# Kernel tuning notes

Measured on AMD Instinct MI355X. Metric: run time of the kernel, lower is better.

## Reference

```python
import jax, jax.numpy as jnp
import numpy as np

B, T, D, M = 2048, 512, 8, 2  # groups, timesteps, state_rank, n_measures


def setup_inputs() -> dict:
    key = jax.random.key(0)
    ks = jax.random.split(key, 7)
    inp = jax.random.normal(ks[0], (B, T, M), dtype=jnp.float32)
    mean0 = 0.1 * jax.random.normal(ks[1], (B, D), dtype=jnp.float32)
    A = 0.1 * jax.random.normal(ks[2], (B, D, D), dtype=jnp.float32)
    cov0 = A @ jnp.swapaxes(A, -1, -2) + jnp.eye(D, dtype=jnp.float32)  # PSD initial cov
    F = 0.95 * jnp.eye(D, dtype=jnp.float32) + 0.01 * jax.random.normal(ks[3], (D, D), dtype=jnp.float32)
    H = jax.random.normal(ks[4], (M, D), dtype=jnp.float32)
    Aq = 0.1 * jax.random.normal(ks[5], (D, D), dtype=jnp.float32)
    Q = Aq @ Aq.T + 0.1 * jnp.eye(D, dtype=jnp.float32)
    Ar = 0.1 * jax.random.normal(ks[6], (M, M), dtype=jnp.float32)
    R = Ar @ Ar.T + 0.1 * jnp.eye(M, dtype=jnp.float32)
    return dict(input=inp, mean0=mean0, cov0=cov0, F=F, H=H, Q=Q, R=R)


def _kf_scan(input, mean0, cov0, F, H, Q, R):
    """n_step=1 Kalman recurrence: at t emit the 1-step-ahead prediction made
    from data up to t-1 (so output[0] is the initial state), matching
    ScriptKalmanFilter.forward with n_step=1."""

    def step(carry, x_t):
        mean, cov = carry  # [B,D], [B,D,D]
        # --- update ---
        HP = jnp.einsum('md,bde->bme', H, cov)                 # H P : [B,M,D]
        S = jnp.einsum('bme,ne->bmn', HP, H) + R               # innovation cov [B,M,M]
        Kt = jnp.linalg.solve(S, HP)                           # K^T = S^{-1} H P : [B,M,D]
        resid = x_t - jnp.einsum('md,bd->bm', H, mean)         # [B,M]
        mean_u = mean + jnp.einsum('bmd,bm->bd', Kt, resid)
        cov_u = cov - jnp.einsum('bmd,bme->bde', Kt, HP)       # (I-KH)P
        # --- predict ---
        mean_p = jnp.einsum('de,be->bd', F, mean_u)
        cov_p = jnp.einsum('de,bef,gf->bdg', F, cov_u, F) + Q  # F P F^T + Q
        return (mean_p, cov_p), (mean_p, cov_p)

    xs = jnp.swapaxes(input, 0, 1)  # [T,B,M]
    _, (means_s, covs_s) = jax.lax.scan(step, (mean0, cov0), xs)
    # output at step t is the state BEFORE consuming x_t (1-step-ahead)
    means = jnp.concatenate([mean0[None], means_s[:-1]], axis=0)  # [T,B,D]
    covs = jnp.concatenate([cov0[None], covs_s[:-1]], axis=0)     # [T,B,D,D]
    return jnp.swapaxes(means, 0, 1), jnp.swapaxes(covs, 0, 1)


def reference(input, mean0, cov0, F, H, Q, R):
    means, covs = _kf_scan(input, mean0, cov0, F, H, Q, R)
    b, t, m = input.shape
    Rs = jnp.broadcast_to(R, (b, t, m, m))      # stacked per-time R (static design)
    Hs = jnp.broadcast_to(H, (b, t, m, H.shape[-1]))
    return means, covs, Rs, Hs
```

## Files before the change

### kernel.cpp

```cpp
#include <hip/hip_runtime.h>

typedef float v2 __attribute__((ext_vector_type(2)));
typedef float v4 __attribute__((ext_vector_type(4)));

#define B_TOT 2048
#define T_STEPS 512

#define OFF_COVS 8388608
#define OFF_RS   75497472
#define OFF_HS   79691776

__launch_bounds__(64, 1)
__global__ void kf_kernel(const float* __restrict__ input,
                          const float* __restrict__ mean0,
                          const float* __restrict__ cov0,
                          const float* __restrict__ Fm,
                          const float* __restrict__ Hm,
                          const float* __restrict__ Qm,
                          const float* __restrict__ Rm,
                          float* __restrict__ out)
{
    __shared__ float xs[8 * 1024];
    __shared__ float hp0_s[8 * 12];
    __shared__ float hp1_s[8 * 12];
    __shared__ float mean_s[8 * 12];
    __shared__ float u_s[8 * 88];

    const int lane = threadIdx.x;
    const int g = lane >> 3;
    const int j = lane & 7;
    const int b0 = blockIdx.x * 8;
    const int b = b0 + g;

    {
        const v4* src = (const v4*)(input + (size_t)b0 * 1024);
        v4* dst = (v4*)xs;
        #pragma unroll
        for (int i = 0; i < 32; ++i)
            dst[i * 64 + lane] = src[i * 64 + lane];
    }

    v2 Fcol2[8][4];
    #pragma unroll
    for (int f = 0; f < 8; ++f)
        #pragma unroll
        for (int d2 = 0; d2 < 4; ++d2) {
            v2 t; t.x = Fm[(2 * d2) * 8 + f]; t.y = Fm[(2 * d2 + 1) * 8 + f];
            Fcol2[f][d2] = t;
        }
    v2 Frowj[4];
    #pragma unroll
    for (int d2 = 0; d2 < 4; ++d2) {
        v2 t; t.x = Fm[j * 8 + 2 * d2]; t.y = Fm[j * 8 + 2 * d2 + 1];
        Frowj[d2] = t;
    }
    v2 Hrow2[2][4];
    #pragma unroll
    for (int m = 0; m < 2; ++m)
        #pragma unroll
        for (int d2 = 0; d2 < 4; ++d2) {
            v2 t; t.x = Hm[m * 8 + 2 * d2]; t.y = Hm[m * 8 + 2 * d2 + 1];
            Hrow2[m][d2] = t;
        }
    v2 HFrow2[2][4];
    #pragma unroll
    for (int m = 0; m < 2; ++m)
        #pragma unroll
        for (int d2 = 0; d2 < 4; ++d2) {
            float a = 0.f, c = 0.f;
            #pragma unroll
            for (int k = 0; k < 8; ++k) {
                a += Hm[m * 8 + k] * Fm[k * 8 + 2 * d2];
                c += Hm[m * 8 + k] * Fm[k * 8 + 2 * d2 + 1];
            }
            v2 t; t.x = a; t.y = c; HFrow2[m][d2] = t;
        }
    v2 Qrow2[4];
    #pragma unroll
    for (int e2 = 0; e2 < 4; ++e2) {
        v2 t; t.x = Qm[j * 8 + 2 * e2]; t.y = Qm[j * 8 + 2 * e2 + 1];
        Qrow2[e2] = t;
    }
    const float r00 = Rm[0], r01 = Rm[1], r10 = Rm[2], r11 = Rm[3];
    const float Rval = (j == 0) ? r00 : (j == 1) ? r01 : (j == 2) ? r10 : r11;
    v2 Hflat; Hflat.x = Hm[2 * j]; Hflat.y = Hm[2 * j + 1];

    v2 P2[4];
    {
        const v4* c4 = (const v4*)(cov0 + (size_t)b * 64 + j * 8);
        v4 a = c4[0], bb = c4[1];
        P2[0].x = a.x;  P2[0].y = a.y;  P2[1].x = a.z;  P2[1].y = a.w;
        P2[2].x = bb.x; P2[2].y = bb.y; P2[3].x = bb.z; P2[3].y = bb.w;
    }
    float mean_j = mean0[(size_t)b * 8 + j];

    float hm0, hm1;
    mean_s[g * 12 + j] = mean_j;
    __syncthreads();
    {
        const v4* ms = (const v4*)(mean_s + g * 12);
        v4 a = ms[0], bb = ms[1];
        v2 mu[4];
        mu[0].x = a.x;  mu[0].y = a.y;  mu[1].x = a.z;  mu[1].y = a.w;
        mu[2].x = bb.x; mu[2].y = bb.y; mu[3].x = bb.z; mu[3].y = bb.w;
        v2 t0 = {0.f, 0.f}, t1 = {0.f, 0.f};
        #pragma unroll
        for (int d2 = 0; d2 < 4; ++d2) { t0 += Hrow2[0][d2] * mu[d2]; t1 += Hrow2[1][d2] * mu[d2]; }
        hm0 = t0.x + t0.y; hm1 = t1.x + t1.y;
    }

    float* means_p = out + (size_t)b * T_STEPS * 8 + j;
    float* covs_p  = out + OFF_COVS + (size_t)b * T_STEPS * 64 + j * 8;
    float* Rs_p    = out + OFF_RS + (size_t)b * T_STEPS * 4 + j;
    float* Hs_p    = out + OFF_HS + (size_t)b * T_STEPS * 16 + 2 * j;
    const v2* xv   = (const v2*)(xs + g * 1024);

    for (int t = 0; t < T_STEPS; ++t) {
        means_p[0] = mean_j;
        {
            v4 cva, cvb;
            cva.x = P2[0].x; cva.y = P2[0].y; cva.z = P2[1].x; cva.w = P2[1].y;
            cvb.x = P2[2].x; cvb.y = P2[2].y; cvb.z = P2[3].x; cvb.w = P2[3].y;
            ((v4*)covs_p)[0] = cva;
            ((v4*)covs_p)[1] = cvb;
        }
        if (j < 4) Rs_p[0] = Rval;
        *((v2*)Hs_p) = Hflat;
        means_p += 8; covs_p += 64; Rs_p += 4; Hs_p += 16;

        v2 a0 = {0.f, 0.f}, a1 = {0.f, 0.f};
        #pragma unroll
        for (int d2 = 0; d2 < 4; ++d2) { a0 += Hrow2[0][d2] * P2[d2]; a1 += Hrow2[1][d2] * P2[d2]; }
        const float hp0 = a0.x + a0.y;
        const float hp1 = a1.x + a1.y;
        hp0_s[g * 12 + j] = hp0;
        hp1_s[g * 12 + j] = hp1;
        __syncthreads();

        v2 hpa0[4], hpa1[4];
        {
            const v2* p0 = (const v2*)(hp0_s + g * 12);
            const v2* p1 = (const v2*)(hp1_s + g * 12);
            #pragma unroll
            for (int f2 = 0; f2 < 4; ++f2) { hpa0[f2] = p0[f2]; hpa1[f2] = p1[f2]; }
        }

        v2 s00v = {0.f, 0.f}, s01v = {0.f, 0.f}, s11v = {0.f, 0.f};
        #pragma unroll
        for (int f2 = 0; f2 < 4; ++f2) {
            s00v += hpa0[f2] * Hrow2[0][f2];
            s01v += hpa0[f2] * Hrow2[1][f2];
            s11v += hpa1[f2] * Hrow2[1][f2];
        }
        const float s00 = s00v.x + s00v.y + r00;
        const float s01 = s01v.x + s01v.y + r01;
        const float s11 = s11v.x + s11v.y + r11;
        const float det = s00 * s11 - s01 * s01;
        const float idet = __builtin_amdgcn_rcpf(det);
        const float i00 = s11 * idet, i01 = -s01 * idet, i11 = s00 * idet;
        const float kt0 = i00 * hp0 + i01 * hp1;
        const float kt1 = i01 * hp0 + i11 * hp1;

        const v2 x = xv[t];
        const float rs0 = x.x - hm0;
        const float rs1 = x.y - hm1;
        const float mean_u = mean_j + kt0 * rs0 + kt1 * rs1;

        v2 cu[4];
        {
            v2 k0; k0.x = kt0; k0.y = kt0;
            v2 k1; k1.x = kt1; k1.y = kt1;
            #pragma unroll
            for (int f2 = 0; f2 < 4; ++f2)
                cu[f2] = P2[f2] - k0 * hpa0[f2] - k1 * hpa1[f2];
        }

        v2 u2[4] = {{0.f, 0.f}, {0.f, 0.f}, {0.f, 0.f}, {0.f, 0.f}};
        #pragma unroll
        for (int f = 0; f < 8; ++f) {
            const float cuf = (f & 1) ? cu[f >> 1].y : cu[f >> 1].x;
            v2 c; c.x = cuf; c.y = cuf;
            #pragma unroll
            for (int d2 = 0; d2 < 4; ++d2) u2[d2] += Fcol2[f][d2] * c;
        }

        mean_s[g * 12 + j] = mean_u;
        #pragma unroll
        for (int d = 0; d < 8; ++d) {
            const float ud = (d & 1) ? u2[d >> 1].y : u2[d >> 1].x;
            u_s[g * 88 + d * 10 + j] = ud;
        }
        __syncthreads();

        v2 ur[4];
        {
            const v2* up = (const v2*)(u_s + g * 88 + j * 10);
            #pragma unroll
            for (int f2 = 0; f2 < 4; ++f2) ur[f2] = up[f2];
        }
        v2 mu2[4];
        {
            const v4* ms = (const v4*)(mean_s + g * 12);
            v4 a = ms[0], bb = ms[1];
            mu2[0].x = a.x;  mu2[0].y = a.y;  mu2[1].x = a.z;  mu2[1].y = a.w;
            mu2[2].x = bb.x; mu2[2].y = bb.y; mu2[3].x = bb.z; mu2[3].y = bb.w;
        }

        v2 Pn[4] = {Qrow2[0], Qrow2[1], Qrow2[2], Qrow2[3]};
        #pragma unroll
        for (int f = 0; f < 8; ++f) {
            const float uf = (f & 1) ? ur[f >> 1].y : ur[f >> 1].x;
            v2 c; c.x = uf; c.y = uf;
            #pragma unroll
            for (int e2 = 0; e2 < 4; ++e2) Pn[e2] += Fcol2[f][e2] * c;
        }
        P2[0] = Pn[0]; P2[1] = Pn[1]; P2[2] = Pn[2]; P2[3] = Pn[3];

        v2 t0 = {0.f, 0.f}, t1 = {0.f, 0.f}, t2 = {0.f, 0.f};
        #pragma unroll
        for (int d2 = 0; d2 < 4; ++d2) {
            t0 += Frowj[d2] * mu2[d2];
            t1 += HFrow2[0][d2] * mu2[d2];
            t2 += HFrow2[1][d2] * mu2[d2];
        }
        mean_j = t0.x + t0.y;
        hm0 = t1.x + t1.y;
        hm1 = t2.x + t2.y;
    }
}

extern "C" void kernel_launch(void* const* d_in, const int* in_sizes, int n_in,
                              void* d_out, int out_size, void* d_ws, size_t ws_size,
                              hipStream_t stream) {
    const float* input = (const float*)d_in[0];
    const float* mean0 = (const float*)d_in[1];
    const float* cov0  = (const float*)d_in[2];
    const float* F     = (const float*)d_in[3];
    const float* H     = (const float*)d_in[4];
    const float* Q     = (const float*)d_in[5];
    const float* R     = (const float*)d_in[6];
    float* out = (float*)d_out;

    hipLaunchKernelGGL(kf_kernel, dim3(B_TOT / 8), dim3(64), 0, stream,
                       input, mean0, cov0, F, H, Q, R, out);
}
```

Baseline: 581.6 us.

## Reassociate covariance predict to compute F·P early and drop per-step barriers

```diff
diff --git a/kernel.cpp b/kernel.cpp
--- a/kernel.cpp
+++ b/kernel.cpp
@@ -9,6 +9,8 @@
 #define OFF_COVS 8388608
 #define OFF_RS   75497472
 #define OFF_HS   79691776
+
+static __device__ __forceinline__ v2 sp(float s) { v2 r; r.x = s; r.y = s; return r; }
 
 __launch_bounds__(64, 1)
 __global__ void kf_kernel(const float* __restrict__ input,
@@ -21,10 +23,9 @@
                           float* __restrict__ out)
 {
     __shared__ float xs[8 * 1024];
-    __shared__ float hp0_s[8 * 12];
-    __shared__ float hp1_s[8 * 12];
+    __shared__ float hps[8 * 28];
+    __shared__ float ws[8 * 84];
     __shared__ float mean_s[8 * 12];
-    __shared__ float u_s[8 * 88];
 
     const int lane = threadIdx.x;
     const int g = lane >> 3;
@@ -96,7 +97,6 @@
 
     float hm0, hm1;
     mean_s[g * 12 + j] = mean_j;
-    __syncthreads();
     {
         const v4* ms = (const v4*)(mean_s + g * 12);
         v4 a = ms[0], bb = ms[1];
@@ -115,7 +115,31 @@
     float* Hs_p    = out + OFF_HS + (size_t)b * T_STEPS * 16 + 2 * j;
     const v2* xv   = (const v2*)(xs + g * 1024);
 
+    v2 xcur = xv[0];
+
     for (int t = 0; t < T_STEPS; ++t) {
+        v2 a0 = {0.f, 0.f}, a1 = {0.f, 0.f};
+        #pragma unroll
+        for (int d2 = 0; d2 < 4; ++d2) { a0 += Hrow2[0][d2] * P2[d2]; a1 += Hrow2[1][d2] * P2[d2]; }
+        const float hp0 = a0.x + a0.y;
+        const float hp1 = a1.x + a1.y;
+        hps[g * 28 + j]      = hp0;
+        hps[g * 28 + 10 + j] = hp1;
+
+        v2 W2[4] = {{0.f,0.f},{0.f,0.f},{0.f,0.f},{0.f,0.f}};
+        #pragma unroll
+        for (int f = 0; f < 8; ++f) {
+            const float pf = (f & 1) ? P2[f >> 1].y : P2[f >> 1].x;
+            const v2 c = sp(pf);
+            #pragma unroll
+            for (int d2 = 0; d2 < 4; ++d2) W2[d2] += Fcol2[f][d2] * c;
+        }
+        #pragma unroll
+        for (int d = 0; d < 8; ++d) {
+            const float wd = (d & 1) ? W2[d >> 1].y : W2[d >> 1].x;
+            ws[g * 84 + d * 10 + j] = wd;
+        }
+
         means_p[0] = mean_j;
         {
             v4 cva, cvb;
@@ -128,19 +152,12 @@
         *((v2*)Hs_p) = Hflat;
         means_p += 8; covs_p += 64; Rs_p += 4; Hs_p += 16;
 
-        v2 a0 = {0.f, 0.f}, a1 = {0.f, 0.f};
-        #pragma unroll
-        for (int d2 = 0; d2 < 4; ++d2) { a0 += Hrow2[0][d2] * P2[d2]; a1 += Hrow2[1][d2] * P2[d2]; }
-        const float hp0 = a0.x + a0.y;
-        const float hp1 = a1.x + a1.y;
-        hp0_s[g * 12 + j] = hp0;
-        hp1_s[g * 12 + j] = hp1;
-        __syncthreads();
+        const v2 xnext = xv[(t + 1) & (T_STEPS - 1)];
 
         v2 hpa0[4], hpa1[4];
         {
-            const v2* p0 = (const v2*)(hp0_s + g * 12);
-            const v2* p1 = (const v2*)(hp1_s + g * 12);
+            const v2* p0 = (const v2*)(hps + g * 28);
+            const v2* p1 = (const v2*)(hps + g * 28 + 10);
             #pragma unroll
             for (int f2 = 0; f2 < 4; ++f2) { hpa0[f2] = p0[f2]; hpa1[f2] = p1[f2]; }
         }
@@ -158,45 +175,31 @@
         const float det = s00 * s11 - s01 * s01;
         const float idet = __builtin_amdgcn_rcpf(det);
         const float i00 = s11 * idet, i01 = -s01 * idet, i11 = s00 * idet;
+
         const float kt0 = i00 * hp0 + i01 * hp1;
         const float kt1 = i01 * hp0 + i11 * hp1;
-
-        const v2 x = xv[t];
-        const float rs0 = x.x - hm0;
-        const float rs1 = x.y - hm1;
+        const float rs0 = xcur.x - hm0;
+        const float rs1 = xcur.y - hm1;
         const float mean_u = mean_j + kt0 * rs0 + kt1 * rs1;
-
-        v2 cu[4];
-        {
-            v2 k0; k0.x = kt0; k0.y = kt0;
-            v2 k1; k1.x = kt1; k1.y = kt1;
-            #pragma unroll
-            for (int f2 = 0; f2 < 4; ++f2)
-                cu[f2] = P2[f2] - k0 * hpa0[f2] - k1 * hpa1[f2];
-        }
-
-        v2 u2[4] = {{0.f, 0.f}, {0.f, 0.f}, {0.f, 0.f}, {0.f, 0.f}};
-        #pragma unroll
-        for (int f = 0; f < 8; ++f) {
-            const float cuf = (f & 1) ? cu[f >> 1].y : cu[f >> 1].x;
-            v2 c; c.x = cuf; c.y = cuf;
-            #pragma unroll
-            for (int d2 = 0; d2 < 4; ++d2) u2[d2] += Fcol2[f][d2] * c;
-        }
-
         mean_s[g * 12 + j] = mean_u;
-        #pragma unroll
-        for (int d = 0; d < 8; ++d) {
-            const float ud = (d & 1) ? u2[d >> 1].y : u2[d >> 1].x;
-            u_s[g * 88 + d * 10 + j] = ud;
-        }
-        __syncthreads();
-
-        v2 ur[4];
-        {
-            const v2* up = (const v2*)(u_s + g * 88 + j * 10);
-            #pragma unroll
-            for (int f2 = 0; f2 < 4; ++f2) ur[f2] = up[f2];
+
+        v2 dd0 = {0.f, 0.f}, dd1 = {0.f, 0.f};
+        #pragma unroll
+        for (int f2 = 0; f2 < 4; ++f2) { dd0 += Frowj[f2] * hpa0[f2]; dd1 += Frowj[f2] * hpa1[f2]; }
+        const float d0 = dd0.x + dd0.y;
+        const float d1 = dd1.x + dd1.y;
+        const float c0 = i00 * d0 + i01 * d1;
+        const float c1 = i01 * d0 + i11 * d1;
+        const v2 c0v = sp(c0), c1v = sp(c1);
+        v2 z[4];
+        #pragma unroll
+        for (int f2 = 0; f2 < 4; ++f2) z[f2] = c0v * hpa0[f2] + c1v * hpa1[f2];
+
+        v2 Wr[4];
+        {
+            const v2* wp = (const v2*)(ws + g * 84 + j * 10);
+            #pragma unroll
+            for (int f2 = 0; f2 < 4; ++f2) Wr[f2] = wp[f2];
         }
         v2 mu2[4];
         {
@@ -206,11 +209,14 @@
             mu2[2].x = bb.x; mu2[2].y = bb.y; mu2[3].x = bb.z; mu2[3].y = bb.w;
         }
 
+        v2 Wt[4];
+        #pragma unroll
+        for (int f2 = 0; f2 < 4; ++f2) Wt[f2] = Wr[f2] - z[f2];
         v2 Pn[4] = {Qrow2[0], Qrow2[1], Qrow2[2], Qrow2[3]};
         #pragma unroll
         for (int f = 0; f < 8; ++f) {
-            const float uf = (f & 1) ? ur[f >> 1].y : ur[f >> 1].x;
-            v2 c; c.x = uf; c.y = uf;
+            const float wtf = (f & 1) ? Wt[f >> 1].y : Wt[f >> 1].x;
+            const v2 c = sp(wtf);
             #pragma unroll
             for (int e2 = 0; e2 < 4; ++e2) Pn[e2] += Fcol2[f][e2] * c;
         }
@@ -226,6 +232,7 @@
         mean_j = t0.x + t0.y;
         hm0 = t1.x + t1.y;
         hm1 = t2.x + t2.y;
+        xcur = xnext;
     }
 }
 
```

Result: no change. 588.1 us (+1.1%).
